# Kernel optimization log

Hardware: AMD Instinct MI355X
Metric: run time of the kernel (lower is better)

## Reference

```python
import jax, jax.numpy as jnp
import numpy as np

N = 100_000   # nodes
E = 3_200_000 # edges
K = 3         # num_stacks
T = 4         # num_layers (shared weights)
H = 16        # hidden channels of conv1
EPS = 1e-5    # BatchNorm eps


def setup_inputs() -> dict:
    key = jax.random.key(0)
    ks = jax.random.split(key, 12)
    def glorot(k, shape):
        fan = shape[-2] + shape[-1]
        return jax.random.normal(k, shape, jnp.float32) * (2.0 / fan) ** 0.5
    return {
        "x": jax.random.normal(ks[0], (N, 1), jnp.float32),
        "edge_index": jax.random.randint(ks[1], (2, E), 0, N, jnp.int32),
        "edge_weight": jax.random.uniform(ks[2], (E,), jnp.float32),
        # conv1: in=1, out=16  (init_weight [K,Fin,Fout], shared weight [K,Fout,Fout], root [K,Fin,Fout], bias [K,Fout])
        "conv1_init_w": glorot(ks[3], (K, 1, H)),
        "conv1_w": glorot(ks[4], (K, H, H)),
        "conv1_root_w": glorot(ks[5], (K, 1, H)),
        "conv1_bias": jnp.zeros((K, H), jnp.float32),
        # BatchNorm1d(16) in eval mode: running stats + affine params
        "bn1_gamma": jnp.ones((H,), jnp.float32),
        "bn1_beta": jnp.zeros((H,), jnp.float32),
        "bn1_mean": jnp.zeros((H,), jnp.float32),
        "bn1_var": jnp.ones((H,), jnp.float32),
        # conv2: in=16, out=1, act=None
        "conv2_init_w": glorot(ks[6], (K, H, 1)),
        "conv2_w": glorot(ks[7], (K, 1, 1)),
        "conv2_root_w": glorot(ks[8], (K, H, 1)),
        "conv2_bias": jnp.zeros((K, 1), jnp.float32),
    }


def _gcn_norm(edge_index, edge_weight):
    # ARMAConv uses gcn_norm with add_self_loops=False
    row, col = edge_index[0], edge_index[1]
    deg = jax.ops.segment_sum(edge_weight, col, num_segments=N)
    dis = jnp.where(deg > 0, jax.lax.rsqrt(jnp.maximum(deg, 1e-12)), 0.0)
    norm = dis[row] * edge_weight * dis[col]
    return row, col, norm


def _arma(x, row, col, norm, init_w, w, root_w, bias, act):
    # x: [N, Fin]; out per stack: [K, N, Fout]
    root = jnp.einsum('nf,kfo->kno', x, root_w) + bias[:, None, :]
    out = jnp.einsum('nf,kfo->kno', x, init_w)
    for t in range(T):
        if t > 0:
            out = jnp.einsum('kno,kop->knp', out, w)  # shared weight
        msg = out[:, row, :] * norm[None, :, None]     # [K, E, F] gather + scale
        out = jax.ops.segment_sum(msg.transpose(1, 0, 2), col, num_segments=N)  # [N, K, F]
        out = out.transpose(1, 0, 2) + root            # scatter-add + skip (root)
        if act:
            out = jax.nn.relu(out)
    return out.mean(axis=0)  # mean over stacks -> [N, Fout]


def reference(x, edge_index, edge_weight,
              conv1_init_w, conv1_w, conv1_root_w, conv1_bias,
              bn1_gamma, bn1_beta, bn1_mean, bn1_var,
              conv2_init_w, conv2_w, conv2_root_w, conv2_bias):
    row, col, norm = _gcn_norm(edge_index, edge_weight)
    h = _arma(x, row, col, norm, conv1_init_w, conv1_w, conv1_root_w, conv1_bias, act=True)
    # BatchNorm1d (eval) + ReLU; dropout is identity in eval
    h = (h - bn1_mean) * jax.lax.rsqrt(bn1_var + EPS) * bn1_gamma + bn1_beta
    h = jax.nn.relu(h)
    h = _arma(h, row, col, norm, conv2_init_w, conv2_w, conv2_root_w, conv2_bias, act=False)
    return jax.nn.sigmoid(h)  # [N, 1]
```

## Files before the change

### kernel.cpp

```cpp
#include <hip/hip_runtime.h>
#include <math.h>

#define NN 100000
#define NE 3200000
#define NBUCK 782
#define EPB 4096
#define NBLK 782
#define SB_Q 16
#define SCAP 4608
#define BN_EPS 1e-5f

static inline size_t alignup(size_t v) { return (v + 255) & ~size_t(255); }

__device__ inline unsigned short f2bf(float x) {
  unsigned u = __float_as_uint(x);
  u += 0x7FFF + ((u >> 16) & 1);
  return (unsigned short)(u >> 16);
}
__device__ inline float bf2f(unsigned short h) {
  return __uint_as_float((unsigned)h << 16);
}
__device__ inline float edgew(int e) {
  return __uint_as_float((unsigned)e & 0xFFFE0000u);
}

__global__ void k_hist(const int* __restrict__ col, int* __restrict__ cntm) {
  __shared__ int cnt[NBUCK];
  for (int i = threadIdx.x; i < NBUCK; i += 256) cnt[i] = 0;
  __syncthreads();
  int e0 = blockIdx.x * EPB;
  int nE = min(EPB, NE - e0);
  for (int i = threadIdx.x; i < nE; i += 256) atomicAdd(&cnt[col[e0 + i] >> 7], 1);
  __syncthreads();
  int* dst = cntm + (size_t)blockIdx.x * NBUCK;
  for (int i = threadIdx.x; i < NBUCK; i += 256) dst[i] = cnt[i];
}

__global__ void k_scanb(const int* __restrict__ cntm, int* __restrict__ basem,
                        int* __restrict__ btot) {
  __shared__ int s[NBLK][SB_Q + 1];
  int q0 = blockIdx.x * SB_Q;
  int nq = min(SB_Q, NBUCK - q0);
  int t = threadIdx.x;
  for (int idx = t; idx < NBLK * SB_Q; idx += 256) {
    int i = idx >> 4, j = idx & 15;
    s[i][j] = (j < nq) ? cntm[(size_t)i * NBUCK + q0 + j] : 0;
  }
  __syncthreads();
  int wave = t >> 6, lane = t & 63;
  for (int j = wave; j < SB_Q; j += 4) {
    int carry = 0;
    for (int c = 0; c < (NBLK + 63) / 64; ++c) {
      int i = c * 64 + lane;
      int v = (i < NBLK) ? s[i][j] : 0;
      int x = v;
      #pragma unroll
      for (int d = 1; d < 64; d <<= 1) {
        int tt = __shfl_up(x, d, 64);
        if (lane >= d) x += tt;
      }
      if (i < NBLK) s[i][j] = x - v + carry;
      carry += __shfl(x, 63, 64);
    }
    if (lane == 0 && j < nq) btot[q0 + j] = carry;
  }
  __syncthreads();
  for (int idx = t; idx < NBLK * SB_Q; idx += 256) {
    int i = idx >> 4, j = idx & 15;
    if (j < nq) basem[(size_t)i * NBUCK + q0 + j] = s[i][j];
  }
}

__global__ void k_scanq(const int* __restrict__ btot, int* __restrict__ gbase) {
  __shared__ int s[NBUCK];
  __shared__ int c[256];
  const int NCH = (NBUCK + 3) / 4;
  int t = threadIdx.x;
  for (int i = t; i < NBUCK; i += 256) s[i] = btot[i];
  __syncthreads();
  if (t < NCH) {
    int b0 = 4 * t, sum = 0;
    #pragma unroll
    for (int j = 0; j < 4; ++j) if (b0 + j < NBUCK) sum += s[b0 + j];
    c[t] = sum;
  }
  __syncthreads();
  for (int d = 1; d < NCH; d <<= 1) {
    int v = (t < NCH && t >= d) ? c[t - d] : 0;
    __syncthreads();
    if (t < NCH) c[t] += v;
    __syncthreads();
  }
  if (t < NCH) {
    int b0 = 4 * t;
    int run = (t > 0) ? c[t - 1] : 0;
    #pragma unroll
    for (int j = 0; j < 4; ++j)
      if (b0 + j < NBUCK) { int v = s[b0 + j]; s[b0 + j] = run; run += v; }
  }
  __syncthreads();
  for (int i = t; i < NBUCK; i += 256) gbase[i] = s[i];
}

__global__ void k_scat(const int* __restrict__ row, const int* __restrict__ col,
                       const float* __restrict__ ew, const int* __restrict__ basem,
                       const int* __restrict__ gbase, int2* __restrict__ bin) {
  __shared__ int segB[NBUCK];
  __shared__ int cnt[NBUCK];
  __shared__ int csc[256];
  __shared__ int2 stage[EPB];
  __shared__ unsigned short qarr[EPB];
  int b = blockIdx.x, t = threadIdx.x;
  for (int i = t; i < NBUCK; i += 256) {
    segB[i] = gbase[i] + basem[(size_t)b * NBUCK + i];
    cnt[i] = 0;
  }
  __syncthreads();
  int e0 = b * EPB;
  int nE = min(EPB, NE - e0);
  for (int i = t; i < nE; i += 256) atomicAdd(&cnt[col[e0 + i] >> 7], 1);
  __syncthreads();
  const int NCH = (NBUCK + 3) / 4;
  int q4 = 4 * t;
  if (t < NCH) {
    int sum = 0;
    #pragma unroll
    for (int j = 0; j < 4; ++j) if (q4 + j < NBUCK) sum += cnt[q4 + j];
    csc[t] = sum;
  }
  __syncthreads();
  for (int d = 1; d < NCH; d <<= 1) {
    int v = (t < NCH && t >= d) ? csc[t - d] : 0;
    __syncthreads();
    if (t < NCH) csc[t] += v;
    __syncthreads();
  }
  if (t < NCH) {
    int run = (t > 0) ? csc[t - 1] : 0;
    #pragma unroll
    for (int j = 0; j < 4; ++j)
      if (q4 + j < NBUCK) {
        int v = cnt[q4 + j];
        segB[q4 + j] -= run;
        cnt[q4 + j] = run;
        run += v;
      }
  }
  __syncthreads();
  for (int i = t; i < nE; i += 256) {
    int e = e0 + i;
    int cc = col[e], q = cc >> 7;
    int p = atomicAdd(&cnt[q], 1);
    stage[p] = make_int2(row[e] | ((cc & 127) << 17), __float_as_int(ew[e]));
    qarr[p] = (unsigned short)q;
  }
  __syncthreads();
  for (int p = t; p < nE; p += 256) {
    int q = qarr[p];
    bin[segB[q] + p] = stage[p];
  }
}

__global__ void k_build(const int* __restrict__ gbase, const int* __restrict__ btot,
                        const int2* __restrict__ bin,
                        int* __restrict__ csr, float* __restrict__ dis,
                        int* __restrict__ nstart, int* __restrict__ ncnt) {
  __shared__ int2 stage[SCAP];
  __shared__ int cnt[128];
  __shared__ float degw[128];
  __shared__ int off[129];
  int b = blockIdx.x;
  int gb0 = gbase[b];
  int nb = btot[b];
  const int2* gb = bin + gb0;
  for (int i = threadIdx.x; i < 128; i += 256) { cnt[i] = 0; degw[i] = 0.f; }
  __syncthreads();
  for (int i = threadIdx.x; i < nb; i += 256) {
    int2 v = gb[i];
    if (i < SCAP) stage[i] = v;
    int c = (v.x >> 17) & 127;
    atomicAdd(&cnt[c], 1);
    atomicAdd(&degw[c], __int_as_float(v.y));
  }
  __syncthreads();
  if (threadIdx.x == 0) {
    int s = 0;
    for (int c = 0; c < 128; ++c) { off[c] = s; s += cnt[c]; }
    off[128] = s;
  }
  __syncthreads();
  for (int c = threadIdx.x; c < 128; c += 256) {
    int n = b * 128 + c;
    if (n < NN) {
      nstart[n] = gb0 + off[c];
      ncnt[n] = cnt[c];
      float d = degw[c];
      dis[n] = (d > 0.f) ? rsqrtf(fmaxf(d, 1e-12f)) : 0.f;
    }
  }
  __syncthreads();
  for (int i = threadIdx.x; i < 128; i += 256) cnt[i] = 0;
  __syncthreads();
  int* cb = csr + gb0;
  for (int i = threadIdx.x; i < nb; i += 256) {
    int2 v = (i < SCAP) ? stage[i] : gb[i];
    int c = (v.x >> 17) & 127;
    int pos = off[c] + atomicAdd(&cnt[c], 1);
    unsigned u = (unsigned)v.y;
    u += 0xFFFFu + ((u >> 17) & 1);
    cb[pos] = (v.x & 0x1FFFF) | (int)(u & 0xFFFE0000u);
  }
}

__global__ void k_init1(const float* __restrict__ x, const float* __restrict__ rw,
                        const float* __restrict__ bias, const float* __restrict__ dis,
                        unsigned short* __restrict__ root1, float* __restrict__ s) {
  int idx = blockIdx.x * 256 + threadIdx.x;
  if (idx >= NN * 16) return;
  int n = idx >> 4, f = idx & 15;
  float xv = x[n];
  if (f == 0) s[n] = dis[n] * xv;
  root1[n * 48 + f]      = f2bf(xv * rw[f]      + bias[f]);
  root1[n * 48 + 16 + f] = f2bf(xv * rw[16 + f] + bias[16 + f]);
  root1[n * 48 + 32 + f] = f2bf(xv * rw[32 + f] + bias[32 + f]);
}

__global__ void k_prop_first(const float* __restrict__ s,
                             const unsigned short* __restrict__ root,
                             ushort4* __restrict__ outp, const int* __restrict__ csr,
                             const int* __restrict__ nstart, const int* __restrict__ ncnt,
                             const float* __restrict__ dis, const float* __restrict__ w,
                             const float* __restrict__ iw) {
  __shared__ float ws[768];
  for (int i = threadIdx.x; i < 768; i += 256) ws[i] = w[i];
  __syncthreads();
  int f = threadIdx.x & 15;
  int n = (blockIdx.x * 256 + threadIdx.x) >> 4;
  if (n >= NN) return;
  int e0 = nstart[n], cnt = ncnt[n];
  float g = 0.f;
  for (int i = f; i < cnt; i += 16) {
    int e = csr[e0 + i];
    g = fmaf(edgew(e), s[e & 0x1FFFF], g);
  }
  #pragma unroll
  for (int d = 8; d; d >>= 1) g += __shfl_xor(g, d, 16);
  float dn = dis[n];
  float dg = dn * g;
  float a0 = fmaxf(fmaf(dg, iw[f],      bf2f(root[n * 48 + f])),      0.f);
  float a1 = fmaxf(fmaf(dg, iw[16 + f], bf2f(root[n * 48 + 16 + f])), 0.f);
  float a2 = fmaxf(fmaf(dg, iw[32 + f], bf2f(root[n * 48 + 32 + f])), 0.f);
  float n0 = 0.f, n1 = 0.f, n2 = 0.f;
  #pragma unroll
  for (int f2 = 0; f2 < 16; ++f2) {
    float b0 = __shfl(a0, f2, 16);
    float b1 = __shfl(a1, f2, 16);
    float b2v = __shfl(a2, f2, 16);
    n0 = fmaf(b0, ws[f2 * 16 + f], n0);
    n1 = fmaf(b1, ws[256 + f2 * 16 + f], n1);
    n2 = fmaf(b2v, ws[512 + f2 * 16 + f], n2);
  }
  ushort4 pk;
  pk.x = f2bf(dn * n0); pk.y = f2bf(dn * n1); pk.z = f2bf(dn * n2); pk.w = 0;
  outp[(size_t)n * 16 + f] = pk;
}

template <bool APPLY_W>
__global__ void k_prop16(const ushort4* __restrict__ in,
                         const unsigned short* __restrict__ root,
                         ushort4* __restrict__ outp, const int* __restrict__ csr,
                         const int* __restrict__ nstart, const int* __restrict__ ncnt,
                         const float* __restrict__ dis, const float* __restrict__ w,
                         const float* __restrict__ bng, const float* __restrict__ bnb,
                         const float* __restrict__ bnm, const float* __restrict__ bnv,
                         const float* __restrict__ iw2, const float* __restrict__ rw2,
                         const float* __restrict__ b2,
                         float4* __restrict__ root2, float4* __restrict__ o2) {
  __shared__ float ws[768];
  if (APPLY_W) {
    for (int i = threadIdx.x; i < 768; i += 256) ws[i] = w[i];
    __syncthreads();
  }
  int f = threadIdx.x & 15;
  int n = (blockIdx.x * 256 + threadIdx.x) >> 4;
  if (n >= NN) return;
  int e0 = nstart[n], cnt = ncnt[n];
  float a0 = 0.f, a1 = 0.f, a2 = 0.f;
  int i = 0;
  for (; i + 16 <= cnt; i += 16) {
    int e[16];
    ushort4 v[16];
    #pragma unroll
    for (int j = 0; j < 16; ++j) e[j] = csr[e0 + i + j];
    #pragma unroll
    for (int j = 0; j < 16; ++j) v[j] = in[(size_t)(e[j] & 0x1FFFF) * 16 + f];
    #pragma unroll
    for (int j = 0; j < 16; ++j) {
      float we = edgew(e[j]);
      a0 = fmaf(we, bf2f(v[j].x), a0);
      a1 = fmaf(we, bf2f(v[j].y), a1);
      a2 = fmaf(we, bf2f(v[j].z), a2);
    }
  }
  for (; i + 8 <= cnt; i += 8) {
    int e[8];
    ushort4 v[8];
    #pragma unroll
    for (int j = 0; j < 8; ++j) e[j] = csr[e0 + i + j];
    #pragma unroll
    for (int j = 0; j < 8; ++j) v[j] = in[(size_t)(e[j] & 0x1FFFF) * 16 + f];
    #pragma unroll
    for (int j = 0; j < 8; ++j) {
      float we = edgew(e[j]);
      a0 = fmaf(we, bf2f(v[j].x), a0);
      a1 = fmaf(we, bf2f(v[j].y), a1);
      a2 = fmaf(we, bf2f(v[j].z), a2);
    }
  }
  for (; i + 4 <= cnt; i += 4) {
    int e[4];
    ushort4 v[4];
    #pragma unroll
    for (int j = 0; j < 4; ++j) e[j] = csr[e0 + i + j];
    #pragma unroll
    for (int j = 0; j < 4; ++j) v[j] = in[(size_t)(e[j] & 0x1FFFF) * 16 + f];
    #pragma unroll
    for (int j = 0; j < 4; ++j) {
      float we = edgew(e[j]);
      a0 = fmaf(we, bf2f(v[j].x), a0);
      a1 = fmaf(we, bf2f(v[j].y), a1);
      a2 = fmaf(we, bf2f(v[j].z), a2);
    }
  }
  for (; i < cnt; ++i) {
    int e = csr[e0 + i];
    float we = edgew(e);
    ushort4 v = in[(size_t)(e & 0x1FFFF) * 16 + f];
    a0 = fmaf(we, bf2f(v.x), a0);
    a1 = fmaf(we, bf2f(v.y), a1);
    a2 = fmaf(we, bf2f(v.z), a2);
  }
  float dn = dis[n];
  a0 = fmaxf(fmaf(dn, a0, bf2f(root[n * 48 + f])),      0.f);
  a1 = fmaxf(fmaf(dn, a1, bf2f(root[n * 48 + 16 + f])), 0.f);
  a2 = fmaxf(fmaf(dn, a2, bf2f(root[n * 48 + 32 + f])), 0.f);
  if (APPLY_W) {
    float n0 = 0.f, n1 = 0.f, n2 = 0.f;
    #pragma unroll
    for (int f2 = 0; f2 < 16; ++f2) {
      float b0 = __shfl(a0, f2, 16);
      float b1 = __shfl(a1, f2, 16);
      float b2v = __shfl(a2, f2, 16);
      n0 = fmaf(b0, ws[f2 * 16 + f], n0);
      n1 = fmaf(b1, ws[256 + f2 * 16 + f], n1);
      n2 = fmaf(b2v, ws[512 + f2 * 16 + f], n2);
    }
    ushort4 pk;
    pk.x = f2bf(dn * n0); pk.y = f2bf(dn * n1); pk.z = f2bf(dn * n2); pk.w = 0;
    outp[(size_t)n * 16 + f] = pk;
  } else {
    float mean = (a0 + a1 + a2) * (1.f / 3.f);
    float hv = fmaxf((mean - bnm[f]) * rsqrtf(bnv[f] + BN_EPS) * bng[f] + bnb[f], 0.f);
    float d0 = hv * iw2[f],      r0 = hv * rw2[f];
    float d1 = hv * iw2[16 + f], r1 = hv * rw2[16 + f];
    float d2 = hv * iw2[32 + f], r2 = hv * rw2[32 + f];
    #pragma unroll
    for (int d = 8; d; d >>= 1) {
      d0 += __shfl_xor(d0, d, 16); r0 += __shfl_xor(r0, d, 16);
      d1 += __shfl_xor(d1, d, 16); r1 += __shfl_xor(r1, d, 16);
      d2 += __shfl_xor(d2, d, 16); r2 += __shfl_xor(r2, d, 16);
    }
    if (f == 0) {
      float4 rt, oo;
      rt.x = r0 + b2[0]; rt.y = r1 + b2[1]; rt.z = r2 + b2[2]; rt.w = 0.f;
      oo.x = dn * d0; oo.y = dn * d1; oo.z = dn * d2; oo.w = 0.f;
      root2[n] = rt;
      o2[n] = oo;
    }
  }
}

template <bool LAST>
__global__ void k_prop1(const float4* __restrict__ in, const float4* __restrict__ root,
                        float4* __restrict__ outp, float* __restrict__ outf,
                        const int* __restrict__ csr,
                        const int* __restrict__ nstart, const int* __restrict__ ncnt,
                        const float* __restrict__ dis, const float* __restrict__ w2) {
  int lane = threadIdx.x & 15;
  int n = (blockIdx.x * 256 + threadIdx.x) >> 4;
  if (n >= NN) return;
  int e0 = nstart[n], cnt = ncnt[n];
  float a0 = 0.f, a1 = 0.f, a2 = 0.f;
  for (int i = lane; i < cnt; i += 16) {
    int e = csr[e0 + i];
    float we = edgew(e);
    float4 src = in[e & 0x1FFFF];
    a0 = fmaf(we, src.x, a0);
    a1 = fmaf(we, src.y, a1);
    a2 = fmaf(we, src.z, a2);
  }
  #pragma unroll
  for (int d = 8; d; d >>= 1) {
    a0 += __shfl_xor(a0, d, 16);
    a1 += __shfl_xor(a1, d, 16);
    a2 += __shfl_xor(a2, d, 16);
  }
  if (lane == 0) {
    float dn = dis[n];
    float4 rt = root[n];
    if (LAST) {
      float s = fmaf(dn, a0, rt.x) + fmaf(dn, a1, rt.y) + fmaf(dn, a2, rt.z);
      s *= (1.f / 3.f);
      outf[n] = 1.f / (1.f + expf(-s));
    } else {
      float4 oo;
      oo.x = dn * fmaf(dn, a0, rt.x) * w2[0];
      oo.y = dn * fmaf(dn, a1, rt.y) * w2[1];
      oo.z = dn * fmaf(dn, a2, rt.z) * w2[2];
      oo.w = 0.f;
      outp[n] = oo;
    }
  }
}

extern "C" void kernel_launch(void* const* d_in, const int* in_sizes, int n_in,
                              void* d_out, int out_size, void* d_ws, size_t ws_size,
                              hipStream_t stream) {
  const float* x     = (const float*)d_in[0];
  const int*   ei    = (const int*)d_in[1];
  const float* ew    = (const float*)d_in[2];
  const float* c1_iw = (const float*)d_in[3];
  const float* c1_w  = (const float*)d_in[4];
  const float* c1_rw = (const float*)d_in[5];
  const float* c1_b  = (const float*)d_in[6];
  const float* bn_g  = (const float*)d_in[7];
  const float* bn_b  = (const float*)d_in[8];
  const float* bn_m  = (const float*)d_in[9];
  const float* bn_v  = (const float*)d_in[10];
  const float* c2_iw = (const float*)d_in[11];
  const float* c2_w  = (const float*)d_in[12];
  const float* c2_rw = (const float*)d_in[13];
  const float* c2_b  = (const float*)d_in[14];
  float* out = (float*)d_out;

  char* p = (char*)d_ws;
  auto take = [&](size_t bytes) -> char* { char* r = p; p += alignup(bytes); return r; };
  int*     cntm   = (int*)take((size_t)NBLK * NBUCK * 4);
  int*     basem  = (int*)take((size_t)NBLK * NBUCK * 4);
  int*     btot   = (int*)take((size_t)NBUCK * 4);
  int*     gbase  = (int*)take((size_t)NBUCK * 4);
  int2*    bin    = (int2*)take((size_t)NE * 8);
  int*     csr    = (int*)take((size_t)NE * 4);
  float*   dis    = (float*)take((size_t)NN * 4);
  int*     nst    = (int*)take((size_t)NN * 4);
  int*     ncn    = (int*)take((size_t)NN * 4);
  unsigned short* root1 = (unsigned short*)take((size_t)NN * 48 * 2);
  float*   sbuf   = (float*)take((size_t)NN * 4);
  ushort4* bufA   = (ushort4*)take((size_t)NN * 16 * 8);
  ushort4* bufB   = (ushort4*)take((size_t)NN * 16 * 8);
  float4*  root2  = (float4*)take((size_t)NN * 16);
  float4*  o2A    = (float4*)take((size_t)NN * 16);
  float4*  o2B    = (float4*)take((size_t)NN * 16);

  const int* row = ei;
  const int* col = ei + NE;

  const int gP = (NN * 16 + 255) / 256;
  const int gSB = (NBUCK + SB_Q - 1) / SB_Q;

  k_hist <<<NBLK, 256, 0, stream>>>(col, cntm);
  k_scanb<<<gSB, 256, 0, stream>>>(cntm, basem, btot);
  k_scanq<<<1, 256, 0, stream>>>(btot, gbase);
  k_scat <<<NBLK, 256, 0, stream>>>(row, col, ew, basem, gbase, bin);
  k_build<<<NBUCK, 256, 0, stream>>>(gbase, btot, bin, csr, dis, nst, ncn);

  k_init1<<<gP, 256, 0, stream>>>(x, c1_rw, c1_b, dis, root1, sbuf);
  k_prop_first<<<gP, 256, 0, stream>>>(sbuf, root1, bufA, csr, nst, ncn, dis, c1_w, c1_iw);
  k_prop16<true ><<<gP, 256, 0, stream>>>(bufA, root1, bufB, csr, nst, ncn, dis, c1_w,
      nullptr, nullptr, nullptr, nullptr, nullptr, nullptr, nullptr, nullptr, nullptr);
  k_prop16<true ><<<gP, 256, 0, stream>>>(bufB, root1, bufA, csr, nst, ncn, dis, c1_w,
      nullptr, nullptr, nullptr, nullptr, nullptr, nullptr, nullptr, nullptr, nullptr);
  k_prop16<false><<<gP, 256, 0, stream>>>(bufA, root1, nullptr, csr, nst, ncn, dis, nullptr,
      bn_g, bn_b, bn_m, bn_v, c2_iw, c2_rw, c2_b, root2, o2A);

  k_prop1<false><<<gP, 256, 0, stream>>>(o2A, root2, o2B, nullptr, csr, nst, ncn, dis, c2_w);
  k_prop1<false><<<gP, 256, 0, stream>>>(o2B, root2, o2A, nullptr, csr, nst, ncn, dis, c2_w);
  k_prop1<false><<<gP, 256, 0, stream>>>(o2A, root2, o2B, nullptr, csr, nst, ncn, dis, c2_w);
  k_prop1<true ><<<gP, 256, 0, stream>>>(o2B, root2, nullptr, out, csr, nst, ncn, dis, c2_w);
}
```

Baseline: 393.3 us.

## Reuse histogram via prefix diff, store conv2 features in bf16, add launch bounds

k_scat no longer recomputes the per-block bucket histogram with shared atomics. It derives the counts as the difference of consecutive rows of the exclusive-scan matrix, with a sentinel row of totals appended by k_scanb. Conv2's intermediate per-node features (o2 buffers) are packed as bf16 ushort4 instead of float4, halving gather bytes in k_prop1. k_prop16 also gets launch bounds for higher occupancy and drops the 8-wide remainder loop. The bf16 storage adds rounding error in the second ARMA layer.

```diff
diff --git a/kernel.cpp b/kernel.cpp
--- a/kernel.cpp
+++ b/kernel.cpp
@@ -62,7 +62,10 @@
       if (i < NBLK) s[i][j] = x - v + carry;
       carry += __shfl(x, 63, 64);
     }
-    if (lane == 0 && j < nq) btot[q0 + j] = carry;
+    if (lane == 0 && j < nq) {
+      btot[q0 + j] = carry;
+      basem[(size_t)NBLK * NBUCK + q0 + j] = carry;
+    }
   }
   __syncthreads();
   for (int idx = t; idx < NBLK * SB_Q; idx += 256) {
@@ -111,14 +114,13 @@
   __shared__ int2 stage[EPB];
   __shared__ unsigned short qarr[EPB];
   int b = blockIdx.x, t = threadIdx.x;
+  const int* rowA = basem + (size_t)b * NBUCK;
+  const int* rowB = basem + (size_t)(b + 1) * NBUCK;
   for (int i = t; i < NBUCK; i += 256) {
-    segB[i] = gbase[i] + basem[(size_t)b * NBUCK + i];
-    cnt[i] = 0;
-  }
-  __syncthreads();
-  int e0 = b * EPB;
-  int nE = min(EPB, NE - e0);
-  for (int i = t; i < nE; i += 256) atomicAdd(&cnt[col[e0 + i] >> 7], 1);
+    int a = rowA[i];
+    segB[i] = gbase[i] + a;
+    cnt[i] = rowB[i] - a;
+  }
   __syncthreads();
   const int NCH = (NBUCK + 3) / 4;
   int q4 = 4 * t;
@@ -147,6 +149,8 @@
       }
   }
   __syncthreads();
+  int e0 = b * EPB;
+  int nE = min(EPB, NE - e0);
   for (int i = t; i < nE; i += 256) {
     int e = e0 + i;
     int cc = col[e], q = cc >> 7;
@@ -266,16 +270,17 @@
 }
 
 template <bool APPLY_W>
-__global__ void k_prop16(const ushort4* __restrict__ in,
-                         const unsigned short* __restrict__ root,
-                         ushort4* __restrict__ outp, const int* __restrict__ csr,
-                         const int* __restrict__ nstart, const int* __restrict__ ncnt,
-                         const float* __restrict__ dis, const float* __restrict__ w,
-                         const float* __restrict__ bng, const float* __restrict__ bnb,
-                         const float* __restrict__ bnm, const float* __restrict__ bnv,
-                         const float* __restrict__ iw2, const float* __restrict__ rw2,
-                         const float* __restrict__ b2,
-                         float4* __restrict__ root2, float4* __restrict__ o2) {
+__global__ __launch_bounds__(256, 6)
+void k_prop16(const ushort4* __restrict__ in,
+              const unsigned short* __restrict__ root,
+              ushort4* __restrict__ outp, const int* __restrict__ csr,
+              const int* __restrict__ nstart, const int* __restrict__ ncnt,
+              const float* __restrict__ dis, const float* __restrict__ w,
+              const float* __restrict__ bng, const float* __restrict__ bnb,
+              const float* __restrict__ bnm, const float* __restrict__ bnv,
+              const float* __restrict__ iw2, const float* __restrict__ rw2,
+              const float* __restrict__ b2,
+              float4* __restrict__ root2, ushort4* __restrict__ o2) {
   __shared__ float ws[768];
   if (APPLY_W) {
     for (int i = threadIdx.x; i < 768; i += 256) ws[i] = w[i];
@@ -302,21 +307,6 @@
       a2 = fmaf(we, bf2f(v[j].z), a2);
     }
   }
-  for (; i + 8 <= cnt; i += 8) {
-    int e[8];
-    ushort4 v[8];
-    #pragma unroll
-    for (int j = 0; j < 8; ++j) e[j] = csr[e0 + i + j];
-    #pragma unroll
-    for (int j = 0; j < 8; ++j) v[j] = in[(size_t)(e[j] & 0x1FFFF) * 16 + f];
-    #pragma unroll
-    for (int j = 0; j < 8; ++j) {
-      float we = edgew(e[j]);
-      a0 = fmaf(we, bf2f(v[j].x), a0);
-      a1 = fmaf(we, bf2f(v[j].y), a1);
-      a2 = fmaf(we, bf2f(v[j].z), a2);
-    }
-  }
   for (; i + 4 <= cnt; i += 4) {
     int e[4];
     ushort4 v[4];
@@ -371,18 +361,19 @@
       d2 += __shfl_xor(d2, d, 16); r2 += __shfl_xor(r2, d, 16);
     }
     if (f == 0) {
-      float4 rt, oo;
+      float4 rt;
       rt.x = r0 + b2[0]; rt.y = r1 + b2[1]; rt.z = r2 + b2[2]; rt.w = 0.f;
-      oo.x = dn * d0; oo.y = dn * d1; oo.z = dn * d2; oo.w = 0.f;
       root2[n] = rt;
-      o2[n] = oo;
+      ushort4 pk;
+      pk.x = f2bf(dn * d0); pk.y = f2bf(dn * d1); pk.z = f2bf(dn * d2); pk.w = 0;
+      o2[n] = pk;
     }
   }
 }
 
 template <bool LAST>
-__global__ void k_prop1(const float4* __restrict__ in, const float4* __restrict__ root,
-                        float4* __restrict__ outp, float* __restrict__ outf,
+__global__ void k_prop1(const ushort4* __restrict__ in, const float4* __restrict__ root,
+                        ushort4* __restrict__ outp, float* __restrict__ outf,
                         const int* __restrict__ csr,
                         const int* __restrict__ nstart, const int* __restrict__ ncnt,
                         const float* __restrict__ dis, const float* __restrict__ w2) {
@@ -394,10 +385,10 @@
   for (int i = lane; i < cnt; i += 16) {
     int e = csr[e0 + i];
     float we = edgew(e);
-    float4 src = in[e & 0x1FFFF];
-    a0 = fmaf(we, src.x, a0);
-    a1 = fmaf(we, src.y, a1);
-    a2 = fmaf(we, src.z, a2);
+    ushort4 src = in[e & 0x1FFFF];
+    a0 = fmaf(we, bf2f(src.x), a0);
+    a1 = fmaf(we, bf2f(src.y), a1);
+    a2 = fmaf(we, bf2f(src.z), a2);
   }
   #pragma unroll
   for (int d = 8; d; d >>= 1) {
@@ -413,12 +404,12 @@
       s *= (1.f / 3.f);
       outf[n] = 1.f / (1.f + expf(-s));
     } else {
-      float4 oo;
-      oo.x = dn * fmaf(dn, a0, rt.x) * w2[0];
-      oo.y = dn * fmaf(dn, a1, rt.y) * w2[1];
-      oo.z = dn * fmaf(dn, a2, rt.z) * w2[2];
-      oo.w = 0.f;
-      outp[n] = oo;
+      ushort4 pk;
+      pk.x = f2bf(dn * fmaf(dn, a0, rt.x) * w2[0]);
+      pk.y = f2bf(dn * fmaf(dn, a1, rt.y) * w2[1]);
+      pk.z = f2bf(dn * fmaf(dn, a2, rt.z) * w2[2]);
+      pk.w = 0;
+      outp[n] = pk;
     }
   }
 }
@@ -446,7 +437,7 @@
   char* p = (char*)d_ws;
   auto take = [&](size_t bytes) -> char* { char* r = p; p += alignup(bytes); return r; };
   int*     cntm   = (int*)take((size_t)NBLK * NBUCK * 4);
-  int*     basem  = (int*)take((size_t)NBLK * NBUCK * 4);
+  int*     basem  = (int*)take((size_t)(NBLK + 1) * NBUCK * 4);
   int*     btot   = (int*)take((size_t)NBUCK * 4);
   int*     gbase  = (int*)take((size_t)NBUCK * 4);
   int2*    bin    = (int2*)take((size_t)NE * 8);
@@ -459,8 +450,8 @@
   ushort4* bufA   = (ushort4*)take((size_t)NN * 16 * 8);
   ushort4* bufB   = (ushort4*)take((size_t)NN * 16 * 8);
   float4*  root2  = (float4*)take((size_t)NN * 16);
-  float4*  o2A    = (float4*)take((size_t)NN * 16);
-  float4*  o2B    = (float4*)take((size_t)NN * 16);
+  ushort4* o2A    = (ushort4*)take((size_t)NN * 8);
+  ushort4* o2B    = (ushort4*)take((size_t)NN * 8);
 
   const int* row = ei;
   const int* col = ei + NE;
```

New measurement: 383.5 us. -2.5%, faster.
